# Kernel tuning notes

Measured on AMD Instinct MI355X. Metric: run time of the kernel, lower is better.

The kernel has to match this reference:

```python
import jax, jax.numpy as jnp
from jax import lax
import numpy as np

SMOOTH = 1e-06
NUM_ITER = 40
KSIZE = 3


def _depthwise_avg3(x):
    # x: [B, C, D, H, W]; 3x3x3 box-average depthwise conv, 'same' padding
    C = x.shape[1]
    k = jnp.full((C, 1, KSIZE, KSIZE, KSIZE), 1.0 / (KSIZE ** 3), x.dtype)
    return lax.conv_general_dilated(
        x, k, window_strides=(1, 1, 1), padding='SAME',
        dimension_numbers=('NCDHW', 'OIDHW', 'NCDHW'),
        feature_group_count=C)


def soft_skeletonize_3d(volume, num_iter=NUM_ITER, smooth=SMOOTH):
    volume = jnp.clip(volume, 0.0, 1.0)

    def step(carry, _):
        skel, done = carry
        eroded = jnp.clip(_depthwise_avg3(skel) - smooth, 0.0, 1.0)
        opened = jnp.clip(_depthwise_avg3(eroded), 0.0, 1.0)
        new = skel * (1.0 - opened + smooth)
        new = jnp.where(done, skel, new)  # freeze after early-stop condition
        done = done | (new.sum() < smooth)
        return (new, done), None

    (skel, _), _ = lax.scan(step, (volume, jnp.array(False)), None, length=num_iter)
    return skel


def compute_centerline_dice(pred_skel, target_skel, smooth=SMOOTH):
    B, C = pred_skel.shape[:2]
    pf = pred_skel.reshape(B, C, -1)
    tf = target_skel.reshape(B, C, -1)
    inter = (pf * tf).sum(axis=2)
    return (2.0 * inter + smooth) / (pf.sum(axis=2) + tf.sum(axis=2) + smooth)


def setup_inputs() -> dict:
    key = jax.random.key(0)
    k1, k2 = jax.random.split(key)
    shape = (2, 1, 128, 128, 128)
    predictions = jax.random.normal(k1, shape, dtype=jnp.float32)  # logits, max > 1 triggers sigmoid
    targets = (jax.random.uniform(k2, shape) < 0.1).astype(jnp.float32)  # sparse binary vessel mask
    return {"predictions": predictions, "targets": targets}


def reference(predictions, targets):
    pred_probs = jnp.where(predictions.max() > 1.0,
                           jax.nn.sigmoid(predictions), predictions)
    pred_skel = soft_skeletonize_3d(pred_probs)
    target_skel = soft_skeletonize_3d(targets)
    cl_dice = compute_centerline_dice(pred_skel, target_skel)
    return (1.0 - cl_dice).mean()
```

## Files before the change

kernel.cpp:

```cpp
#include <hip/hip_runtime.h>
#include <math.h>

#define DIM   128
#define NV    (DIM*DIM*DIM)
#define SM    1e-6f
#define NITER 40
#define ACC_OFF  96
#define FLAG_OFF 104
#define BUF_OFF  256
#define YT 20
#define ZC 8

typedef _Float16 half8 __attribute__((ext_vector_type(8)));

__device__ __forceinline__ float c01(float v){ return fminf(fmaxf(v, 0.f), 1.f); }
__device__ __forceinline__ half8 h8z(){ return (half8)(_Float16)0.f; }

__device__ __forceinline__ _Float16 shflh(_Float16 v, int srcLane){
    unsigned short s = __builtin_bit_cast(unsigned short, v);
    int r = __shfl((int)(unsigned)s, srcLane);
    return __builtin_bit_cast(_Float16, (unsigned short)(r & 0xffff));
}

__device__ __forceinline__ half8 rowsum3(half8 h, int x, int lane){
    _Float16 lft = shflh(h[7], lane - 1); if (x == 0)  lft = (_Float16)0.f;
    _Float16 rgt = shflh(h[0], lane + 1); if (x == 15) rgt = (_Float16)0.f;
    half8 shl, shr;
    shl[0] = lft; shr[7] = rgt;
    #pragma unroll
    for (int k = 1; k < 8; ++k) shl[k] = h[k-1];
    #pragma unroll
    for (int k = 0; k < 7; ++k) shr[k] = h[k+1];
    return shl + h + shr;
}

__device__ __forceinline__ half8 hclip01(half8 v){
    const half8 one  = (half8)(_Float16)1.f;
    const half8 zero = (half8)(_Float16)0.f;
    return __builtin_elementwise_max(__builtin_elementwise_min(v, one), zero);
}

__global__ __launch_bounds__(256)
void k_init_meta(float* meta) { meta[threadIdx.x] = 0.0f; }

__global__ __launch_bounds__(256)
void k_flag(const float4* __restrict__ pred, float* __restrict__ meta, int n4) {
    int stride = gridDim.x * blockDim.x;
    bool hit = false;
    for (int i = blockIdx.x * blockDim.x + threadIdx.x; i < n4; i += stride) {
        float4 p = pred[i];
        hit |= (p.x > 1.f) | (p.y > 1.f) | (p.z > 1.f) | (p.w > 1.f);
    }
    if (hit) meta[FLAG_OFF] = 1.0f;
}

__global__ __launch_bounds__(256)
void k_prep(const float* __restrict__ pred, const float* __restrict__ tgt,
            const float* __restrict__ meta, _Float16* __restrict__ outP,
            _Float16* __restrict__ outT) {
    const bool sg = (meta[FLAG_OFF] != 0.0f);
    const int idx = blockIdx.x * blockDim.x + threadIdx.x;
    const int i8 = idx * 8;
    float4 a = *(const float4*)(pred + i8);
    float4 b = *(const float4*)(pred + i8 + 4);
    float pv[8] = {a.x,a.y,a.z,a.w,b.x,b.y,b.z,b.w};
    half8 hp, ht;
    #pragma unroll
    for (int k = 0; k < 8; ++k) {
        float p = pv[k];
        if (sg) p = 1.f / (1.f + __expf(-p));
        hp[k] = (_Float16)c01(p);
    }
    *(half8*)(outP + i8) = hp;
    float4 c = *(const float4*)(tgt + i8);
    float4 d = *(const float4*)(tgt + i8 + 4);
    float tv[8] = {c.x,c.y,c.z,c.w,d.x,d.y,d.z,d.w};
    #pragma unroll
    for (int k = 0; k < 8; ++k) ht[k] = (_Float16)c01(tv[k]);
    *(half8*)(outT + i8) = ht;
}

__global__ __launch_bounds__(320)
void k_step(const _Float16* __restrict__ src, _Float16* __restrict__ dst,
            float* __restrict__ sums, int iter) {
    __shared__ half8 sA[4][YT][17];
    __shared__ half8 sB[4][YT][17];
    __shared__ float sRed[5];

    const int x    = threadIdx.x;
    const int y    = threadIdx.y;
    const int tid  = y * 16 + x;
    const int lane = tid & 63;
    const int ytile = blockIdx.x & 7;
    const int zch   = blockIdx.x >> 3;
    const int vol   = blockIdx.y;
    const int g     = vol >> 1;
    const int z0    = zch * ZC;
    const int gy    = ytile * 16 - 2 + y;
    const bool rowIn = (gy >= 0) && (gy < DIM);
    const bool midY  = (y >= 1) && (y <= 18);
    const bool outY  = (y >= 2) && (y <= 17);

    bool hitv = (lane < iter) && (sums[lane * 2 + g] < SM);
    const bool done = (__ballot(hitv) != 0ull);

    const _Float16* sp = src + (size_t)vol * NV + (size_t)gy * DIM + x * 8;
    _Float16*       dp = dst + (size_t)vol * NV + (size_t)gy * DIM + x * 8;

    const half8 hz = h8z();
    const half8 onev   = (half8)(_Float16)1.f;
    const half8 inv27v = (half8)(_Float16)(1.f/27.f);
    const half8 smv    = (half8)(_Float16)1e-6f;

    half8 vm4 = hz, vm3 = hz, vm2 = hz, vm1 = hz;
    half8 s1 = hz, s2 = hz;
    half8 r2lo = hz, r2hi = hz;
    half8 g1 = hz, g2 = hz;
    float localSum = 0.f;

    auto LD = [&](int P) -> half8 {
        if (rowIn && P >= 0 && P < DIM && P <= z0 + ZC + 1)
            return *(const half8*)(sp + (size_t)P * (DIM * DIM));
        return h8z();
    };

    auto SUM8 = [&](half8 t) -> float {
        _Float16 s01 = t[0] + t[1], s23 = t[2] + t[3];
        _Float16 s45 = t[4] + t[5], s67 = t[6] + t[7];
        return (float)((s01 + s23) + (s45 + s67));
    };

    half8 hvA = LD(z0 - 2), hvB = LD(z0 - 1);

    for (int Z = z0 - 2; Z <= z0 + ZC + 2; Z += 2) {
        const half8 cA = hvA, cB = hvB;

        const bool liveA = (Z     <= z0 + ZC + 1);
        const bool liveB = (Z + 1 <= z0 + ZC + 1);
        const int sa0 = Z & 3, sa1 = (Z + 1) & 3;
        const int sb0 = (Z - 3) & 3, sb1 = (Z - 2) & 3;

        half8 rsA = hz, rsB = hz;
        if (liveA) { rsA = rowsum3(cA, x, lane); sA[sa0][y][x] = rsA; }
        if (liveB) { rsB = rowsum3(cB, x, lane); sA[sa1][y][x] = rsB; }
        sB[sb0][y][x] = r2lo;
        sB[sb1][y][x] = r2hi;
        __syncthreads();

        hvA = LD(Z + 2); hvB = LD(Z + 3);

        const int ym = (y > 0) ? y - 1 : 0;
        const int yp = (y < YT - 1) ? y + 1 : YT - 1;

        half8 e2lo, e2hi;
        {
            half8 eu = sB[sb0][ym][x], ed = sB[sb0][yp][x];
            e2lo = eu + r2lo + ed;
            half8 fu = sB[sb1][ym][x], fd = sB[sb1][yp][x];
            e2hi = fu + r2hi + fd;
        }

        half8 r2nlo = hz, r2nhi = hz;
        if (liveA) {
            half8 u = sA[sa0][ym][x], d = sA[sa0][yp][x];
            half8 sd = u + rsA + d;
            half8 er = hz;
            if (midY && rowIn && (Z - 1) >= 0 && (Z - 1) < DIM)
                er = hclip01((s2 + s1 + sd) * inv27v - smv);
            s2 = s1; s1 = sd;
            r2nlo = rowsum3(er, x, lane);
        }
        if (liveB) {
            half8 u = sA[sa1][ym][x], d = sA[sa1][yp][x];
            half8 sd = u + rsB + d;
            half8 er = hz;
            if (midY && rowIn && Z >= 0 && Z < DIM)
                er = hclip01((s2 + s1 + sd) * inv27v - smv);
            s2 = s1; s1 = sd;
            r2nhi = rowsum3(er, x, lane);
        }

        const int zoA = Z - 4, zoB = Z - 3;
        if (outY && zoA >= z0) {
            half8 op = __builtin_elementwise_min((g2 + g1 + e2lo) * inv27v, onev);
            half8 nv = done ? vm4 : (half8)(vm4 * (onev - op));
            *(half8*)(dp + (size_t)zoA * (DIM * DIM)) = nv;
            localSum += SUM8(nv);
        }
        if (outY && zoB >= z0) {
            half8 op = __builtin_elementwise_min((g1 + e2lo + e2hi) * inv27v, onev);
            half8 nv = done ? vm3 : (half8)(vm3 * (onev - op));
            *(half8*)(dp + (size_t)zoB * (DIM * DIM)) = nv;
            localSum += SUM8(nv);
        }

        g2 = e2lo; g1 = e2hi;
        r2lo = r2nlo; r2hi = r2nhi;
        vm4 = vm2; vm3 = vm1; vm2 = cA; vm1 = cB;
    }

    float s = localSum;
    for (int off = 32; off > 0; off >>= 1) s += __shfl_down(s, off);
    if (lane == 0) sRed[tid >> 6] = s;
    __syncthreads();
    if (tid == 0)
        atomicAdd(&sums[iter * 2 + g], sRed[0] + sRed[1] + sRed[2] + sRed[3] + sRed[4]);
}

__global__ __launch_bounds__(256)
void k_dice(const _Float16* __restrict__ buf, float* __restrict__ acc) {
    __shared__ float sA[4], sB[4], sC[4];
    const int bx = blockIdx.x, by = blockIdx.y;
    const int ytile = bx & 7, zc16 = bx >> 3;
    const int b = by & 1, zq = by >> 1;
    const int y0 = ytile * 16;
    const int z0 = zc16 * 16 + zq * 4;
    const int tid  = threadIdx.x;
    const int lane = tid & 63;
    const int yy = tid >> 4, xg = tid & 15;

    const _Float16* p = buf + (size_t)b * NV;
    const _Float16* t = buf + (size_t)(2 + b) * NV;

    float si = 0.f, spv = 0.f, stv = 0.f;
    #pragma unroll
    for (int zi = 0; zi < 4; ++zi) {
        const size_t off = ((size_t)(z0 + zi) * DIM + (y0 + yy)) * DIM + xg * 8;
        half8 hp = *(const half8*)(p + off);
        half8 ht = *(const half8*)(t + off);
        #pragma unroll
        for (int k = 0; k < 8; ++k) {
            float pv = (float)hp[k], tv = (float)ht[k];
            si += pv * tv; spv += pv; stv += tv;
        }
    }
    for (int off = 32; off > 0; off >>= 1) {
        si  += __shfl_down(si, off);
        spv += __shfl_down(spv, off);
        stv += __shfl_down(stv, off);
    }
    if (lane == 0) { sA[tid >> 6] = si; sB[tid >> 6] = spv; sC[tid >> 6] = stv; }
    __syncthreads();
    if (tid == 0) {
        atomicAdd(&acc[b * 3 + 0], sA[0] + sA[1] + sA[2] + sA[3]);
        atomicAdd(&acc[b * 3 + 1], sB[0] + sB[1] + sB[2] + sB[3]);
        atomicAdd(&acc[b * 3 + 2], sC[0] + sC[1] + sC[2] + sC[3]);
    }
}

__global__ void k_fin(const float* __restrict__ acc, float* __restrict__ out) {
    float loss = 0.0f;
    for (int b = 0; b < 2; ++b) {
        float inter = acc[b * 3 + 0], spv = acc[b * 3 + 1], stv = acc[b * 3 + 2];
        float dice = (2.0f * inter + SM) / (spv + stv + SM);
        loss += 1.0f - dice;
    }
    out[0] = 0.5f * loss;
}

extern "C" void kernel_launch(void* const* d_in, const int* in_sizes, int n_in,
                              void* d_out, int out_size, void* d_ws, size_t ws_size,
                              hipStream_t stream) {
    (void)in_sizes; (void)n_in; (void)out_size; (void)ws_size;
    const float* pred = (const float*)d_in[0];
    const float* tgt  = (const float*)d_in[1];
    float* out  = (float*)d_out;
    float* meta = (float*)d_ws;
    _Float16* bufA = (_Float16*)(meta + BUF_OFF);
    _Float16* bufB = bufA + (size_t)4 * NV;

    k_init_meta<<<dim3(1), dim3(256), 0, stream>>>(meta);
    k_flag<<<dim3(1024), dim3(256), 0, stream>>>((const float4*)pred, meta, 2 * NV / 4);
    k_prep<<<dim3(2 * NV / 8 / 256), dim3(256), 0, stream>>>(
        pred, tgt, meta, bufA, bufA + (size_t)2 * NV);

    dim3 sgrid(8 * (DIM / ZC), 4);
    dim3 sblock(16, YT);
    for (int it = 0; it < NITER; ++it) {
        const _Float16* s = (it & 1) ? bufB : bufA;
        _Float16*       d = (it & 1) ? bufA : bufB;
        k_step<<<sgrid, sblock, 0, stream>>>(s, d, meta, it);
    }

    k_dice<<<dim3(64, 8), dim3(256), 0, stream>>>(bufA, meta + ACC_OFF);
    k_fin<<<dim3(1), dim3(1), 0, stream>>>(meta + ACC_OFF, out);
}
```

Measured before the change: 833.6 us.

## Fuse prep into first step, fold finalize into dice, use lighter barrier

Removes the separate prep kernel by having a specialized first-iteration step kernel read fp32 inputs directly, applying sigmoid and clamp on the fly. The final loss computation is folded into the dice kernel through a last-block-done atomic counter, and the in-loop barrier becomes an inline waitcnt plus s_barrier. This saves two launches and one full-volume fp32 read and fp16 write pass. In exchange the first step reads fp32 halo rows with redundant sigmoid work, and the counter must start at zero, which relies on the init kernel.

```diff
diff --git a/kernel.cpp b/kernel.cpp
--- a/kernel.cpp
+++ b/kernel.cpp
@@ -6,6 +6,7 @@
 #define SM    1e-6f
 #define NITER 40
 #define ACC_OFF  96
+#define CNT_OFF  102
 #define FLAG_OFF 104
 #define BUF_OFF  256
 #define YT 20
@@ -15,6 +16,10 @@
 
 __device__ __forceinline__ float c01(float v){ return fminf(fmaxf(v, 0.f), 1.f); }
 __device__ __forceinline__ half8 h8z(){ return (half8)(_Float16)0.f; }
+
+__device__ __forceinline__ void barrier_lds(){
+    asm volatile("s_waitcnt lgkmcnt(0)\n\ts_barrier" ::: "memory");
+}
 
 __device__ __forceinline__ _Float16 shflh(_Float16 v, int srcLane){
     unsigned short s = __builtin_bit_cast(unsigned short, v);
@@ -54,161 +59,168 @@
     if (hit) meta[FLAG_OFF] = 1.0f;
 }
 
-__global__ __launch_bounds__(256)
-void k_prep(const float* __restrict__ pred, const float* __restrict__ tgt,
-            const float* __restrict__ meta, _Float16* __restrict__ outP,
-            _Float16* __restrict__ outT) {
-    const bool sg = (meta[FLAG_OFF] != 0.0f);
-    const int idx = blockIdx.x * blockDim.x + threadIdx.x;
-    const int i8 = idx * 8;
-    float4 a = *(const float4*)(pred + i8);
-    float4 b = *(const float4*)(pred + i8 + 4);
-    float pv[8] = {a.x,a.y,a.z,a.w,b.x,b.y,b.z,b.w};
-    half8 hp, ht;
-    #pragma unroll
-    for (int k = 0; k < 8; ++k) {
-        float p = pv[k];
-        if (sg) p = 1.f / (1.f + __expf(-p));
-        hp[k] = (_Float16)c01(p);
-    }
-    *(half8*)(outP + i8) = hp;
-    float4 c = *(const float4*)(tgt + i8);
-    float4 d = *(const float4*)(tgt + i8 + 4);
-    float tv[8] = {c.x,c.y,c.z,c.w,d.x,d.y,d.z,d.w};
-    #pragma unroll
-    for (int k = 0; k < 8; ++k) ht[k] = (_Float16)c01(tv[k]);
-    *(half8*)(outT + i8) = ht;
+#define STEP_BODY(LD_EXPR, DONE_EXPR, SUMS_IDX)                                \
+    __shared__ half8 sA[4][YT][17];                                            \
+    __shared__ half8 sB[4][YT][17];                                            \
+    __shared__ float sRed[5];                                                  \
+    const int x    = threadIdx.x;                                              \
+    const int y    = threadIdx.y;                                              \
+    const int tid  = y * 16 + x;                                               \
+    const int lane = tid & 63;                                                 \
+    const int ytile = blockIdx.x & 7;                                          \
+    const int zch   = blockIdx.x >> 3;                                         \
+    const int vol   = blockIdx.y;                                              \
+    const int g     = vol >> 1;                                                \
+    const int z0    = zch * ZC;                                                \
+    const int gy    = ytile * 16 - 2 + y;                                      \
+    const bool rowIn = (gy >= 0) && (gy < DIM);                                \
+    const bool midY  = (y >= 1) && (y <= 18);                                  \
+    const bool outY  = (y >= 2) && (y <= 17);                                  \
+    const bool done  = (DONE_EXPR);                                            \
+    _Float16* dp = dst + (size_t)vol * NV + (size_t)gy * DIM + x * 8;          \
+    const half8 hz = h8z();                                                    \
+    const half8 onev   = (half8)(_Float16)1.f;                                 \
+    const half8 inv27v = (half8)(_Float16)(1.f/27.f);                          \
+    const half8 smv    = (half8)(_Float16)1e-6f;                               \
+    half8 vm4 = hz, vm3 = hz, vm2 = hz, vm1 = hz;                              \
+    half8 s1 = hz, s2 = hz;                                                    \
+    half8 r2lo = hz, r2hi = hz;                                                \
+    half8 g1 = hz, g2 = hz;                                                    \
+    float localSum = 0.f;                                                      \
+    auto SUM8 = [&](half8 t) -> float {                                        \
+        _Float16 a0 = t[0] + t[1], a1 = t[2] + t[3];                           \
+        _Float16 a2 = t[4] + t[5], a3 = t[6] + t[7];                           \
+        return (float)((a0 + a1) + (a2 + a3));                                 \
+    };                                                                         \
+    half8 hvA = LD_EXPR(z0 - 2), hvB = LD_EXPR(z0 - 1);                        \
+    for (int Z = z0 - 2; Z <= z0 + ZC + 2; Z += 2) {                           \
+        const half8 cA = hvA, cB = hvB;                                        \
+        const bool liveA = (Z     <= z0 + ZC + 1);                             \
+        const bool liveB = (Z + 1 <= z0 + ZC + 1);                             \
+        const int sa0 = Z & 3, sa1 = (Z + 1) & 3;                              \
+        const int sb0 = (Z - 3) & 3, sb1 = (Z - 2) & 3;                        \
+        half8 rsA = hz, rsB = hz;                                              \
+        if (liveA) { rsA = rowsum3(cA, x, lane); sA[sa0][y][x] = rsA; }        \
+        if (liveB) { rsB = rowsum3(cB, x, lane); sA[sa1][y][x] = rsB; }        \
+        sB[sb0][y][x] = r2lo;                                                  \
+        sB[sb1][y][x] = r2hi;                                                  \
+        barrier_lds();                                                         \
+        hvA = LD_EXPR(Z + 2); hvB = LD_EXPR(Z + 3);                            \
+        const int ym = (y > 0) ? y - 1 : 0;                                    \
+        const int yp = (y < YT - 1) ? y + 1 : YT - 1;                          \
+        half8 e2lo, e2hi;                                                      \
+        {                                                                      \
+            half8 eu = sB[sb0][ym][x], ed = sB[sb0][yp][x];                    \
+            e2lo = eu + r2lo + ed;                                             \
+            half8 fu = sB[sb1][ym][x], fd = sB[sb1][yp][x];                    \
+            e2hi = fu + r2hi + fd;                                             \
+        }                                                                      \
+        half8 r2nlo = hz, r2nhi = hz;                                          \
+        if (liveA) {                                                           \
+            half8 u = sA[sa0][ym][x], d = sA[sa0][yp][x];                      \
+            half8 sd = u + rsA + d;                                            \
+            half8 er = hz;                                                     \
+            if (midY && rowIn && (Z - 1) >= 0 && (Z - 1) < DIM)                \
+                er = hclip01((s2 + s1 + sd) * inv27v - smv);                   \
+            s2 = s1; s1 = sd;                                                  \
+            r2nlo = rowsum3(er, x, lane);                                      \
+        }                                                                      \
+        if (liveB) {                                                           \
+            half8 u = sA[sa1][ym][x], d = sA[sa1][yp][x];                      \
+            half8 sd = u + rsB + d;                                            \
+            half8 er = hz;                                                     \
+            if (midY && rowIn && Z >= 0 && Z < DIM)                            \
+                er = hclip01((s2 + s1 + sd) * inv27v - smv);                   \
+            s2 = s1; s1 = sd;                                                  \
+            r2nhi = rowsum3(er, x, lane);                                      \
+        }                                                                      \
+        const int zoA = Z - 4, zoB = Z - 3;                                    \
+        if (outY && zoA >= z0) {                                               \
+            half8 op = __builtin_elementwise_min((g2 + g1 + e2lo) * inv27v, onev); \
+            half8 nv = done ? vm4 : (half8)(vm4 * (onev - op));                \
+            *(half8*)(dp + (size_t)zoA * (DIM * DIM)) = nv;                    \
+            localSum += SUM8(nv);                                              \
+        }                                                                      \
+        if (outY && zoB >= z0) {                                               \
+            half8 op = __builtin_elementwise_min((g1 + e2lo + e2hi) * inv27v, onev); \
+            half8 nv = done ? vm3 : (half8)(vm3 * (onev - op));                \
+            *(half8*)(dp + (size_t)zoB * (DIM * DIM)) = nv;                    \
+            localSum += SUM8(nv);                                              \
+        }                                                                      \
+        g2 = e2lo; g1 = e2hi;                                                  \
+        r2lo = r2nlo; r2hi = r2nhi;                                            \
+        vm4 = vm2; vm3 = vm1; vm2 = cA; vm1 = cB;                              \
+    }                                                                          \
+    float s = localSum;                                                        \
+    for (int off = 32; off > 0; off >>= 1) s += __shfl_down(s, off);           \
+    if (lane == 0) sRed[tid >> 6] = s;                                         \
+    __syncthreads();                                                           \
+    if (tid == 0)                                                              \
+        atomicAdd(&sums[(SUMS_IDX) * 2 + g],                                   \
+                  sRed[0] + sRed[1] + sRed[2] + sRed[3] + sRed[4]);
+
+__global__ __launch_bounds__(320)
+void k_step0(const float* __restrict__ pred, const float* __restrict__ tgt,
+             _Float16* __restrict__ dst, float* __restrict__ sums) {
+    {
+        const int vol_ = blockIdx.y;
+        const int ytile_ = blockIdx.x & 7;
+        const int gy_ = ytile_ * 16 - 2 + (int)threadIdx.y;
+        const bool sg = (sums[FLAG_OFF] != 0.0f);
+        const float* in32 = (vol_ < 2) ? (pred + (size_t)vol_ * NV)
+                                       : (tgt + (size_t)(vol_ - 2) * NV);
+        const float* sp32 = in32 + (size_t)gy_ * DIM + threadIdx.x * 8;
+        const bool doSig = sg && (vol_ < 2);
+        const int zmax_ = (blockIdx.x >> 3) * ZC + ZC + 1;
+        const bool rowIn_ = (gy_ >= 0) && (gy_ < DIM);
+
+        auto LDF = [&](int P) -> half8 {
+            half8 h = h8z();
+            if (rowIn_ && P >= 0 && P < DIM && P <= zmax_) {
+                const float* q = sp32 + (size_t)P * (DIM * DIM);
+                float4 a = *(const float4*)q;
+                float4 b = *(const float4*)(q + 4);
+                float pv[8] = {a.x,a.y,a.z,a.w,b.x,b.y,b.z,b.w};
+                #pragma unroll
+                for (int k = 0; k < 8; ++k) {
+                    float p = pv[k];
+                    if (doSig) p = 1.f / (1.f + __expf(-p));
+                    h[k] = (_Float16)c01(p);
+                }
+            }
+            return h;
+        };
+        STEP_BODY(LDF, false, 0)
+    }
 }
 
 __global__ __launch_bounds__(320)
 void k_step(const _Float16* __restrict__ src, _Float16* __restrict__ dst,
             float* __restrict__ sums, int iter) {
-    __shared__ half8 sA[4][YT][17];
-    __shared__ half8 sB[4][YT][17];
-    __shared__ float sRed[5];
-
-    const int x    = threadIdx.x;
-    const int y    = threadIdx.y;
-    const int tid  = y * 16 + x;
-    const int lane = tid & 63;
-    const int ytile = blockIdx.x & 7;
-    const int zch   = blockIdx.x >> 3;
-    const int vol   = blockIdx.y;
-    const int g     = vol >> 1;
-    const int z0    = zch * ZC;
-    const int gy    = ytile * 16 - 2 + y;
-    const bool rowIn = (gy >= 0) && (gy < DIM);
-    const bool midY  = (y >= 1) && (y <= 18);
-    const bool outY  = (y >= 2) && (y <= 17);
-
-    bool hitv = (lane < iter) && (sums[lane * 2 + g] < SM);
-    const bool done = (__ballot(hitv) != 0ull);
-
-    const _Float16* sp = src + (size_t)vol * NV + (size_t)gy * DIM + x * 8;
-    _Float16*       dp = dst + (size_t)vol * NV + (size_t)gy * DIM + x * 8;
-
-    const half8 hz = h8z();
-    const half8 onev   = (half8)(_Float16)1.f;
-    const half8 inv27v = (half8)(_Float16)(1.f/27.f);
-    const half8 smv    = (half8)(_Float16)1e-6f;
-
-    half8 vm4 = hz, vm3 = hz, vm2 = hz, vm1 = hz;
-    half8 s1 = hz, s2 = hz;
-    half8 r2lo = hz, r2hi = hz;
-    half8 g1 = hz, g2 = hz;
-    float localSum = 0.f;
-
-    auto LD = [&](int P) -> half8 {
-        if (rowIn && P >= 0 && P < DIM && P <= z0 + ZC + 1)
-            return *(const half8*)(sp + (size_t)P * (DIM * DIM));
-        return h8z();
-    };
-
-    auto SUM8 = [&](half8 t) -> float {
-        _Float16 s01 = t[0] + t[1], s23 = t[2] + t[3];
-        _Float16 s45 = t[4] + t[5], s67 = t[6] + t[7];
-        return (float)((s01 + s23) + (s45 + s67));
-    };
-
-    half8 hvA = LD(z0 - 2), hvB = LD(z0 - 1);
-
-    for (int Z = z0 - 2; Z <= z0 + ZC + 2; Z += 2) {
-        const half8 cA = hvA, cB = hvB;
-
-        const bool liveA = (Z     <= z0 + ZC + 1);
-        const bool liveB = (Z + 1 <= z0 + ZC + 1);
-        const int sa0 = Z & 3, sa1 = (Z + 1) & 3;
-        const int sb0 = (Z - 3) & 3, sb1 = (Z - 2) & 3;
-
-        half8 rsA = hz, rsB = hz;
-        if (liveA) { rsA = rowsum3(cA, x, lane); sA[sa0][y][x] = rsA; }
-        if (liveB) { rsB = rowsum3(cB, x, lane); sA[sa1][y][x] = rsB; }
-        sB[sb0][y][x] = r2lo;
-        sB[sb1][y][x] = r2hi;
-        __syncthreads();
-
-        hvA = LD(Z + 2); hvB = LD(Z + 3);
-
-        const int ym = (y > 0) ? y - 1 : 0;
-        const int yp = (y < YT - 1) ? y + 1 : YT - 1;
-
-        half8 e2lo, e2hi;
-        {
-            half8 eu = sB[sb0][ym][x], ed = sB[sb0][yp][x];
-            e2lo = eu + r2lo + ed;
-            half8 fu = sB[sb1][ym][x], fd = sB[sb1][yp][x];
-            e2hi = fu + r2hi + fd;
-        }
-
-        half8 r2nlo = hz, r2nhi = hz;
-        if (liveA) {
-            half8 u = sA[sa0][ym][x], d = sA[sa0][yp][x];
-            half8 sd = u + rsA + d;
-            half8 er = hz;
-            if (midY && rowIn && (Z - 1) >= 0 && (Z - 1) < DIM)
-                er = hclip01((s2 + s1 + sd) * inv27v - smv);
-            s2 = s1; s1 = sd;
-            r2nlo = rowsum3(er, x, lane);
-        }
-        if (liveB) {
-            half8 u = sA[sa1][ym][x], d = sA[sa1][yp][x];
-            half8 sd = u + rsB + d;
-            half8 er = hz;
-            if (midY && rowIn && Z >= 0 && Z < DIM)
-                er = hclip01((s2 + s1 + sd) * inv27v - smv);
-            s2 = s1; s1 = sd;
-            r2nhi = rowsum3(er, x, lane);
-        }
-
-        const int zoA = Z - 4, zoB = Z - 3;
-        if (outY && zoA >= z0) {
-            half8 op = __builtin_elementwise_min((g2 + g1 + e2lo) * inv27v, onev);
-            half8 nv = done ? vm4 : (half8)(vm4 * (onev - op));
-            *(half8*)(dp + (size_t)zoA * (DIM * DIM)) = nv;
-            localSum += SUM8(nv);
-        }
-        if (outY && zoB >= z0) {
-            half8 op = __builtin_elementwise_min((g1 + e2lo + e2hi) * inv27v, onev);
-            half8 nv = done ? vm3 : (half8)(vm3 * (onev - op));
-            *(half8*)(dp + (size_t)zoB * (DIM * DIM)) = nv;
-            localSum += SUM8(nv);
-        }
-
-        g2 = e2lo; g1 = e2hi;
-        r2lo = r2nlo; r2hi = r2nhi;
-        vm4 = vm2; vm3 = vm1; vm2 = cA; vm1 = cB;
-    }
-
-    float s = localSum;
-    for (int off = 32; off > 0; off >>= 1) s += __shfl_down(s, off);
-    if (lane == 0) sRed[tid >> 6] = s;
-    __syncthreads();
-    if (tid == 0)
-        atomicAdd(&sums[iter * 2 + g], sRed[0] + sRed[1] + sRed[2] + sRed[3] + sRed[4]);
+    {
+        const int vol_ = blockIdx.y;
+        const int g_ = vol_ >> 1;
+        const int lane_ = ((int)threadIdx.y * 16 + (int)threadIdx.x) & 63;
+        bool hitv = (lane_ < iter) && (sums[lane_ * 2 + g_] < SM);
+        const bool done_ = (__ballot(hitv) != 0ull);
+        const int ytile_ = blockIdx.x & 7;
+        const int gy_ = ytile_ * 16 - 2 + (int)threadIdx.y;
+        const bool rowIn_ = (gy_ >= 0) && (gy_ < DIM);
+        const int zmax_ = (blockIdx.x >> 3) * ZC + ZC + 1;
+        const _Float16* sp = src + (size_t)vol_ * NV + (size_t)gy_ * DIM + threadIdx.x * 8;
+
+        auto LDH = [&](int P) -> half8 {
+            if (rowIn_ && P >= 0 && P < DIM && P <= zmax_)
+                return *(const half8*)(sp + (size_t)P * (DIM * DIM));
+            return h8z();
+        };
+        STEP_BODY(LDH, done_, iter)
+    }
 }
 
 __global__ __launch_bounds__(256)
-void k_dice(const _Float16* __restrict__ buf, float* __restrict__ acc) {
+void k_dice(const _Float16* __restrict__ buf, float* __restrict__ acc,
+            float* __restrict__ out) {
     __shared__ float sA[4], sB[4], sC[4];
     const int bx = blockIdx.x, by = blockIdx.y;
     const int ytile = bx & 7, zc16 = bx >> 3;
@@ -245,17 +257,21 @@
         atomicAdd(&acc[b * 3 + 0], sA[0] + sA[1] + sA[2] + sA[3]);
         atomicAdd(&acc[b * 3 + 1], sB[0] + sB[1] + sB[2] + sB[3]);
         atomicAdd(&acc[b * 3 + 2], sC[0] + sC[1] + sC[2] + sC[3]);
-    }
-}
-
-__global__ void k_fin(const float* __restrict__ acc, float* __restrict__ out) {
-    float loss = 0.0f;
-    for (int b = 0; b < 2; ++b) {
-        float inter = acc[b * 3 + 0], spv = acc[b * 3 + 1], stv = acc[b * 3 + 2];
-        float dice = (2.0f * inter + SM) / (spv + stv + SM);
-        loss += 1.0f - dice;
-    }
-    out[0] = 0.5f * loss;
+        __threadfence();
+        unsigned int old = atomicAdd((unsigned int*)(acc + (CNT_OFF - ACC_OFF)), 1u);
+        if (old == 64u * 8u - 1u) {
+            float loss = 0.f;
+            #pragma unroll
+            for (int bb = 0; bb < 2; ++bb) {
+                float inter = atomicAdd(&acc[bb * 3 + 0], 0.f);
+                float sp_   = atomicAdd(&acc[bb * 3 + 1], 0.f);
+                float st_   = atomicAdd(&acc[bb * 3 + 2], 0.f);
+                float dice = (2.f * inter + SM) / (sp_ + st_ + SM);
+                loss += 1.f - dice;
+            }
+            out[0] = 0.5f * loss;
+        }
+    }
 }
 
 extern "C" void kernel_launch(void* const* d_in, const int* in_sizes, int n_in,
@@ -271,17 +287,15 @@
 
     k_init_meta<<<dim3(1), dim3(256), 0, stream>>>(meta);
     k_flag<<<dim3(1024), dim3(256), 0, stream>>>((const float4*)pred, meta, 2 * NV / 4);
-    k_prep<<<dim3(2 * NV / 8 / 256), dim3(256), 0, stream>>>(
-        pred, tgt, meta, bufA, bufA + (size_t)2 * NV);
 
     dim3 sgrid(8 * (DIM / ZC), 4);
     dim3 sblock(16, YT);
-    for (int it = 0; it < NITER; ++it) {
+    k_step0<<<sgrid, sblock, 0, stream>>>(pred, tgt, bufB, meta);
+    for (int it = 1; it < NITER; ++it) {
         const _Float16* s = (it & 1) ? bufB : bufA;
         _Float16*       d = (it & 1) ? bufA : bufB;
         k_step<<<sgrid, sblock, 0, stream>>>(s, d, meta, it);
     }
 
-    k_dice<<<dim3(64, 8), dim3(256), 0, stream>>>(bufA, meta + ACC_OFF);
-    k_fin<<<dim3(1), dim3(1), 0, stream>>>(meta + ACC_OFF, out);
-}
+    k_dice<<<dim3(64, 8), dim3(256), 0, stream>>>(bufA, meta + ACC_OFF, out);
+}
```

After: 843.4 us. About the same (+1.2%).
